# Performance work log

Measured on AMD Instinct MI355X. Metric: run time of the kernel, lower is better.

## Reference

```python
import jax, jax.numpy as jnp
import numpy as np


def setup_inputs() -> dict:
    key = jax.random.key(0)
    k1, k2, k3, k4, k5, k6 = jax.random.split(key, 6)
    B, S, IN, OUT = 16, 2048, 1024, 4096
    bound_w = 1.0 / np.sqrt(IN)  # kaiming_uniform-ish scale; values don't affect math
    x = jax.random.normal(k1, (B, S, IN), dtype=jnp.float32)
    weight = jax.random.normal(k2, (OUT, IN), dtype=jnp.float32) * bound_w
    bias = jax.random.normal(k3, (OUT,), dtype=jnp.float32) * bound_w
    prev_weight_grad = jax.random.normal(k4, (OUT, IN), dtype=jnp.float32) * 0.01
    prev_bias_grad = jax.random.normal(k5, (OUT,), dtype=jnp.float32) * 0.01
    batch_lr_samples = jax.random.uniform(k6, (B,), dtype=jnp.float32, minval=1e-8, maxval=1.0)
    return {
        "x": x,
        "weight": weight,
        "bias": bias,
        "prev_weight_grad": prev_weight_grad,
        "prev_bias_grad": prev_bias_grad,
        "batch_lr_samples": batch_lr_samples,
    }


def reference(x, weight, bias, prev_weight_grad, prev_bias_grad, batch_lr_samples):
    # Training-mode forward of OptimizedLinear.
    # simulated_weight[b] = W - lr_b * prevGrad    -> shape [B, out, in]
    lr = batch_lr_samples  # [B]
    simulated_weight = weight[None, :, :] - prev_weight_grad[None, :, :] * lr[:, None, None]
    out = jnp.einsum('bsi,boi->bso', x, simulated_weight)  # [B, S, out]
    simulated_bias = bias[None, :] - prev_bias_grad[None, :] * lr[:, None]  # [B, out]
    out = out + simulated_bias[:, None, :]
    return out
```

## Files before the change

kernel.cpp:

```cpp
#include <hip/hip_runtime.h>
#include <cstdint>
#include <cstddef>

#define PB   16
#define SEQ  2048
#define KIN  1024
#define NOUT 4096

#define BM 256
#define BN 256
#define BK 64
#define NKT (KIN / BK)

typedef __bf16 bf16x8 __attribute__((ext_vector_type(8)));
typedef float  f32x4  __attribute__((ext_vector_type(4)));

__device__ __forceinline__ unsigned short f2bf(float f) {
  union { float f; uint32_t u; } v; v.f = f;
  uint32_t u = v.u;
  u += 0x7fffu + ((u >> 16) & 1u);
  return (unsigned short)(u >> 16);
}

__device__ __forceinline__ void async_copy16(const unsigned short* g, unsigned short* l) {
  __builtin_amdgcn_global_load_lds(
      (const __attribute__((address_space(1))) unsigned int*)g,
      (__attribute__((address_space(3))) unsigned int*)l,
      16, 0, 0);
}

__global__ __launch_bounds__(256) void cvt_x_kernel(const float* __restrict__ x,
                                                    unsigned short* __restrict__ xb) {
  size_t i = ((size_t)blockIdx.x * 256 + threadIdx.x) * 8;
  float4 a = *(const float4*)(x + i);
  float4 b = *(const float4*)(x + i + 4);
  union { unsigned short s[8]; uint4 v; } p;
  p.s[0] = f2bf(a.x); p.s[1] = f2bf(a.y); p.s[2] = f2bf(a.z); p.s[3] = f2bf(a.w);
  p.s[4] = f2bf(b.x); p.s[5] = f2bf(b.y); p.s[6] = f2bf(b.z); p.s[7] = f2bf(b.w);
  *(uint4*)(xb + i) = p.v;
}

__global__ __launch_bounds__(256) void cvt_w_kernel(const float* __restrict__ W,
                                                    const float* __restrict__ G,
                                                    const float* __restrict__ lrs,
                                                    unsigned short* __restrict__ wc) {
  size_t e = ((size_t)blockIdx.x * 256 + threadIdx.x) * 8;
  float4 w0 = *(const float4*)(W + e);
  float4 w1 = *(const float4*)(W + e + 4);
  float4 g0 = *(const float4*)(G + e);
  float4 g1 = *(const float4*)(G + e + 4);
  #pragma unroll
  for (int b = 0; b < PB; ++b) {
    float lr = lrs[b];
    union { unsigned short s[8]; uint4 v; } p;
    p.s[0] = f2bf(w0.x - lr * g0.x); p.s[1] = f2bf(w0.y - lr * g0.y);
    p.s[2] = f2bf(w0.z - lr * g0.z); p.s[3] = f2bf(w0.w - lr * g0.w);
    p.s[4] = f2bf(w1.x - lr * g1.x); p.s[5] = f2bf(w1.y - lr * g1.y);
    p.s[6] = f2bf(w1.z - lr * g1.z); p.s[7] = f2bf(w1.w - lr * g1.w);
    *(uint4*)(wc + (size_t)b * (size_t)NOUT * KIN + e) = p.v;
  }
}

__global__ __launch_bounds__(512, 2) void gemm_kernel(
    const unsigned short* __restrict__ xb,
    const unsigned short* __restrict__ wc,
    const float* __restrict__ bias,
    const float* __restrict__ pbias,
    const float* __restrict__ lrs,
    float* __restrict__ out)
{
  const int tid  = threadIdx.x;
  const int wave = tid >> 6;
  const int lane = tid & 63;
  const int quad = lane >> 4;
  const int l16  = lane & 15;
  const int wm   = wave >> 2;
  const int wn   = wave & 3;

  const int orig = blockIdx.x;
  const int wg   = (orig & 7) * (2048 / 8) + (orig >> 3);
  const int nt = wg & 15;
  const int mt = (wg >> 4) & 7;
  const int b  = wg >> 7;

  __shared__ alignas(16) unsigned short As[2][2][128][64];
  __shared__ alignas(16) unsigned short Bs[2][2][128][64];

  const unsigned short* xA = xb + ((size_t)b * SEQ  + (size_t)mt * BM) * KIN;
  const unsigned short* wB = wc + ((size_t)b * NOUT + (size_t)nt * BN) * KIN;

  const int srow = tid >> 3;
  const int sx   = (tid & 7) ^ (srow & 7);
  const unsigned short* gA = xA + (size_t)srow * KIN + sx * 8;
  const unsigned short* gB = wB + (size_t)srow * KIN + sx * 8;

#define STAGE(d, k0)                                                          \
  do {                                                                        \
    _Pragma("unroll") for (int h = 0; h < 2; ++h) {                           \
      _Pragma("unroll") for (int i = 0; i < 2; ++i) {                         \
        async_copy16(gA + (size_t)(h * 128 + i * 64) * KIN + (k0),            \
                     &As[d][h][i * 64 + wave * 8][0]);                        \
        async_copy16(gB + (size_t)(h * 128 + i * 64) * KIN + (k0),            \
                     &Bs[d][h][i * 64 + wave * 8][0]);                        \
      }                                                                       \
    }                                                                         \
  } while (0)

  const int aoff = l16 * 128;
  const int boff = (wn & 1) * 8192 + l16 * 128;
  const int xs   = (l16 & 7) << 4;
  const int ck0  = (quad * 16) ^ xs;
  const int ck1  = (64 + quad * 16) ^ xs;

  const char* aH0 = (const char*)&As[0][wm][0][0];
  const char* aH1 = (const char*)&As[1][wm][0][0];
  const char* bH0 = (const char*)&Bs[0][wn >> 1][0][0];
  const char* bH1 = (const char*)&Bs[1][wn >> 1][0][0];

  f32x4 acc[8][4];
  #pragma unroll
  for (int i = 0; i < 8; ++i)
    #pragma unroll
    for (int j = 0; j < 4; ++j)
      acc[i][j] = (f32x4){0.f, 0.f, 0.f, 0.f};

#define COMPUTE(AH, BH)                                                       \
  {                                                                           \
    _Pragma("unroll") for (int kk = 0; kk < 2; ++kk) {                        \
      const int ck = kk ? ck1 : ck0;                                          \
      bf16x8 bfr[4];                                                          \
      _Pragma("unroll") for (int mh = 0; mh < 2; ++mh) {                      \
        bf16x8 af[4];                                                         \
        _Pragma("unroll") for (int j = 0; j < 4; ++j)                         \
          af[j] = *(const bf16x8*)((AH) + aoff + (mh * 4 + j) * 2048 + ck);   \
        if (mh == 0) {                                                        \
          _Pragma("unroll") for (int n = 0; n < 4; ++n)                       \
            bfr[n] = *(const bf16x8*)((BH) + boff + n * 2048 + ck);           \
        }                                                                     \
        __builtin_amdgcn_s_barrier();                                         \
        asm volatile("s_waitcnt lgkmcnt(0)" ::: "memory");                    \
        __builtin_amdgcn_sched_barrier(0);                                    \
        __builtin_amdgcn_s_setprio(1);                                        \
        _Pragma("unroll") for (int j = 0; j < 4; ++j)                         \
          _Pragma("unroll") for (int n = 0; n < 4; ++n)                       \
            acc[mh * 4 + j][n] = __builtin_amdgcn_mfma_f32_16x16x32_bf16(     \
                af[j], bfr[n], acc[mh * 4 + j][n], 0, 0, 0);                  \
        __builtin_amdgcn_s_setprio(0);                                        \
        __builtin_amdgcn_sched_barrier(0);                                    \
        __builtin_amdgcn_s_barrier();                                         \
      }                                                                       \
    }                                                                         \
  }

  STAGE(0, 0);
  #pragma unroll 1
  for (int t = 0; t < NKT; t += 2) {
    STAGE(1, (t + 1) * BK);
    asm volatile("s_waitcnt vmcnt(8)" ::: "memory");
    __builtin_amdgcn_sched_barrier(0);
    __builtin_amdgcn_s_barrier();
    COMPUTE(aH0, bH0);
    __builtin_amdgcn_sched_barrier(0);

    if (t + 2 < NKT) {
      STAGE(0, (t + 2) * BK);
      asm volatile("s_waitcnt vmcnt(8)" ::: "memory");
    } else {
      asm volatile("s_waitcnt vmcnt(0)" ::: "memory");
    }
    __builtin_amdgcn_sched_barrier(0);
    __builtin_amdgcn_s_barrier();
    COMPUTE(aH1, bH1);
    __builtin_amdgcn_sched_barrier(0);
  }
#undef STAGE
#undef COMPUTE

  const float lr = lrs[b];
  const int row0 = mt * BM + wm * 128;
  const int col0 = nt * BN + wn * 64;
  float* outB = out + (size_t)b * SEQ * NOUT;
  #pragma unroll
  for (int fn = 0; fn < 4; ++fn) {
    const int o = col0 + fn * 16 + l16;
    const float be = bias[o] - lr * pbias[o];
    #pragma unroll
    for (int fm = 0; fm < 8; ++fm) {
      const int r0 = row0 + fm * 16 + quad * 4;
      #pragma unroll
      for (int r = 0; r < 4; ++r)
        outB[(size_t)(r0 + r) * NOUT + o] = acc[fm][fn][r] + be;
    }
  }
}

extern "C" void kernel_launch(void* const* d_in, const int* in_sizes, int n_in,
                              void* d_out, int out_size, void* d_ws, size_t ws_size,
                              hipStream_t stream) {
  const float* x     = (const float*)d_in[0];
  const float* W     = (const float*)d_in[1];
  const float* bias  = (const float*)d_in[2];
  const float* G     = (const float*)d_in[3];
  const float* pb    = (const float*)d_in[4];
  const float* lrs   = (const float*)d_in[5];
  float* out = (float*)d_out;

  unsigned short* xb = (unsigned short*)d_ws;
  unsigned short* wc = xb + (size_t)PB * SEQ * KIN;

  cvt_x_kernel<<<16384, 256, 0, stream>>>(x, xb);
  cvt_w_kernel<<<2048, 256, 0, stream>>>(W, G, lrs, wc);

  gemm_kernel<<<2048, 512, 0, stream>>>(xb, wc, bias, pb, lrs, out);
}
```

Before: 1.077 ms.

## Split GEMM k-tile into four quarter phases with interleaved async staging

The main loop now processes one k-tile per iteration in four MFMA phases, each over a quarter of the output tile (A-half by B-half). Global-to-LDS copies for the next tiles are issued per quarter and interleaved with those phases, in place of one bulk stage per double-buffer slot. A and B shared-memory tiles are re-laid out so that each wave's rows and columns come from the quarter being computed. The goal is finer overlap of memory traffic with matrix math and more register reuse of A and B fragments across phases. The cost is more barriers per tile and tighter vmcnt ordering that must stay correct.

```diff
diff --git a/kernel.cpp b/kernel.cpp
--- a/kernel.cpp
+++ b/kernel.cpp
@@ -92,30 +92,26 @@
   const int srow = tid >> 3;
   const int sx   = (tid & 7) ^ (srow & 7);
   const unsigned short* gA = xA + (size_t)srow * KIN + sx * 8;
-  const unsigned short* gB = wB + (size_t)srow * KIN + sx * 8;
-
-#define STAGE(d, k0)                                                          \
-  do {                                                                        \
-    _Pragma("unroll") for (int h = 0; h < 2; ++h) {                           \
-      _Pragma("unroll") for (int i = 0; i < 2; ++i) {                         \
-        async_copy16(gA + (size_t)(h * 128 + i * 64) * KIN + (k0),            \
-                     &As[d][h][i * 64 + wave * 8][0]);                        \
-        async_copy16(gB + (size_t)(h * 128 + i * 64) * KIN + (k0),            \
-                     &Bs[d][h][i * 64 + wave * 8][0]);                        \
-      }                                                                       \
-    }                                                                         \
+  const unsigned short* gB = wB + (size_t)(((srow >> 5) * 64) + (srow & 31)) * KIN + sx * 8;
+
+#define STAGE_A(d, mq, k0) do {                                               \
+    async_copy16(gA + (size_t)((mq) * 64) * KIN + (k0),                       \
+                 &As[d][mq][wave * 8][0]);                                    \
+    async_copy16(gA + (size_t)(128 + (mq) * 64) * KIN + (k0),                 \
+                 &As[d][mq][64 + wave * 8][0]);                               \
   } while (0)
-
-  const int aoff = l16 * 128;
-  const int boff = (wn & 1) * 8192 + l16 * 128;
-  const int xs   = (l16 & 7) << 4;
-  const int ck0  = (quad * 16) ^ xs;
-  const int ck1  = (64 + quad * 16) ^ xs;
-
-  const char* aH0 = (const char*)&As[0][wm][0][0];
-  const char* aH1 = (const char*)&As[1][wm][0][0];
-  const char* bH0 = (const char*)&Bs[0][wn >> 1][0][0];
-  const char* bH1 = (const char*)&Bs[1][wn >> 1][0][0];
+#define STAGE_B(d, nq, k0) do {                                               \
+    async_copy16(gB + (size_t)((nq) * 32) * KIN + (k0),                       \
+                 &Bs[d][nq][wave * 8][0]);                                    \
+    async_copy16(gB + (size_t)(128 + (nq) * 32) * KIN + (k0),                 \
+                 &Bs[d][nq][64 + wave * 8][0]);                               \
+  } while (0)
+
+  const int xs    = (l16 & 7) << 4;
+  const int kcol0 = (quad * 16) ^ xs;
+  const int kcol1 = (64 + quad * 16) ^ xs;
+  const int aoff  = (wm * 64 + l16) * 128;
+  const int boff  = (wn * 32 + l16) * 128;
 
   f32x4 acc[8][4];
   #pragma unroll
@@ -124,57 +120,77 @@
     for (int j = 0; j < 4; ++j)
       acc[i][j] = (f32x4){0.f, 0.f, 0.f, 0.f};
 
-#define COMPUTE(AH, BH)                                                       \
+  bf16x8 af[2][4];
+  bf16x8 b0[2][2];
+  bf16x8 b1[2][2];
+
+#define READ_A(c, mq)                                                         \
   {                                                                           \
-    _Pragma("unroll") for (int kk = 0; kk < 2; ++kk) {                        \
-      const int ck = kk ? ck1 : ck0;                                          \
-      bf16x8 bfr[4];                                                          \
-      _Pragma("unroll") for (int mh = 0; mh < 2; ++mh) {                      \
-        bf16x8 af[4];                                                         \
-        _Pragma("unroll") for (int j = 0; j < 4; ++j)                         \
-          af[j] = *(const bf16x8*)((AH) + aoff + (mh * 4 + j) * 2048 + ck);   \
-        if (mh == 0) {                                                        \
-          _Pragma("unroll") for (int n = 0; n < 4; ++n)                       \
-            bfr[n] = *(const bf16x8*)((BH) + boff + n * 2048 + ck);           \
-        }                                                                     \
-        __builtin_amdgcn_s_barrier();                                         \
-        asm volatile("s_waitcnt lgkmcnt(0)" ::: "memory");                    \
-        __builtin_amdgcn_sched_barrier(0);                                    \
-        __builtin_amdgcn_s_setprio(1);                                        \
-        _Pragma("unroll") for (int j = 0; j < 4; ++j)                         \
-          _Pragma("unroll") for (int n = 0; n < 4; ++n)                       \
-            acc[mh * 4 + j][n] = __builtin_amdgcn_mfma_f32_16x16x32_bf16(     \
-                af[j], bfr[n], acc[mh * 4 + j][n], 0, 0, 0);                  \
-        __builtin_amdgcn_s_setprio(0);                                        \
-        __builtin_amdgcn_sched_barrier(0);                                    \
-        __builtin_amdgcn_s_barrier();                                         \
-      }                                                                       \
+    const char* aR = (const char*)&As[c][mq][0][0];                           \
+    _Pragma("unroll") for (int j = 0; j < 4; ++j) {                           \
+      af[0][j] = *(const bf16x8*)(aR + aoff + j * 2048 + kcol0);              \
+      af[1][j] = *(const bf16x8*)(aR + aoff + j * 2048 + kcol1);              \
     }                                                                         \
   }
-
-  STAGE(0, 0);
+#define READ_B(c, nq, BV)                                                     \
+  {                                                                           \
+    const char* bR = (const char*)&Bs[c][nq][0][0];                           \
+    _Pragma("unroll") for (int n = 0; n < 2; ++n) {                           \
+      BV[0][n] = *(const bf16x8*)(bR + boff + n * 2048 + kcol0);              \
+      BV[1][n] = *(const bf16x8*)(bR + boff + n * 2048 + kcol1);              \
+    }                                                                         \
+  }
+#define PHASE_MFMA(AR, AC, BV)                                                \
+  __builtin_amdgcn_s_barrier();                                               \
+  asm volatile("s_waitcnt lgkmcnt(0)" ::: "memory");                          \
+  __builtin_amdgcn_sched_barrier(0);                                          \
+  __builtin_amdgcn_s_setprio(1);                                              \
+  _Pragma("unroll") for (int kk = 0; kk < 2; ++kk)                            \
+    _Pragma("unroll") for (int j = 0; j < 4; ++j)                             \
+      _Pragma("unroll") for (int n = 0; n < 2; ++n)                           \
+        acc[(AR) + j][(AC) + n] = __builtin_amdgcn_mfma_f32_16x16x32_bf16(    \
+            af[kk][j], BV[kk][n], acc[(AR) + j][(AC) + n], 0, 0, 0);          \
+  __builtin_amdgcn_s_setprio(0);                                              \
+  __builtin_amdgcn_s_barrier();
+
+  STAGE_A(0, 0, 0);
+  STAGE_B(0, 0, 0);
+  STAGE_B(0, 1, 0);
+  STAGE_A(0, 1, 0);
+  STAGE_A(1, 0, BK);
+  STAGE_B(1, 0, BK);
+  STAGE_B(1, 1, BK);
+  asm volatile("s_waitcnt vmcnt(6)" ::: "memory");
+  __builtin_amdgcn_sched_barrier(0);
+  __builtin_amdgcn_s_barrier();
+
   #pragma unroll 1
-  for (int t = 0; t < NKT; t += 2) {
-    STAGE(1, (t + 1) * BK);
-    asm volatile("s_waitcnt vmcnt(8)" ::: "memory");
-    __builtin_amdgcn_sched_barrier(0);
-    __builtin_amdgcn_s_barrier();
-    COMPUTE(aH0, bH0);
-    __builtin_amdgcn_sched_barrier(0);
-
+  for (int t = 0; t < NKT; ++t) {
+    const int c = t & 1;
+    if (t + 1 < NKT) STAGE_A(c ^ 1, 1, (t + 1) * BK);
+    READ_A(c, 0);
+    READ_B(c, 0, b0);
+    PHASE_MFMA(0, 0, b0)
+    if (t + 2 < NKT) STAGE_A(c, 0, (t + 2) * BK);
+    READ_B(c, 1, b1);
+    PHASE_MFMA(0, 2, b1)
+    if (t + 2 < NKT) STAGE_B(c, 0, (t + 2) * BK);
+    READ_A(c, 1);
+    PHASE_MFMA(4, 2, b1)
     if (t + 2 < NKT) {
-      STAGE(0, (t + 2) * BK);
-      asm volatile("s_waitcnt vmcnt(8)" ::: "memory");
+      STAGE_B(c, 1, (t + 2) * BK);
+      asm volatile("s_waitcnt vmcnt(6)" ::: "memory");
     } else {
       asm volatile("s_waitcnt vmcnt(0)" ::: "memory");
     }
     __builtin_amdgcn_sched_barrier(0);
-    __builtin_amdgcn_s_barrier();
-    COMPUTE(aH1, bH1);
-    __builtin_amdgcn_sched_barrier(0);
-  }
-#undef STAGE
-#undef COMPUTE
+    PHASE_MFMA(4, 0, b0)
+  }
+#undef STAGE_A
+#undef STAGE_B
+#undef READ_A
+#undef READ_B
+#undef PHASE_MFMA
 
   const float lr = lrs[b];
   const int row0 = mt * BM + wm * 128;
```

New measurement: 1.008 ms. -6.4%, faster.
